# Kernel optimization log

Hardware: AMD Instinct MI355X
Metric: run time of the kernel (lower is better)

The kernel has to match this reference:

```python
import jax, jax.numpy as jnp
import numpy as np

B, T, C = 48, 200, 53          # batch, timepoints, ICA components
E, H, A = 32, 64, 64            # embed dim, GRU hidden dim, attention hidden dim
C2 = C * C                      # 2809
E1 = round(0.05 * C2)           # gta_embed out = 140
E2 = round(0.5 * C2)            # gta_attend hidden = 1404
O = 2                           # output classes
BN_EPS = 1e-5


def setup_inputs() -> dict:
    key = jax.random.key(0)
    ks = jax.random.split(key, 24)
    n = lambda k, shape, s: jax.random.normal(k, shape, dtype=jnp.float32) * s
    return {
        "x": jax.random.normal(ks[0], (B, T, C), dtype=jnp.float32),
        "emb_w": n(ks[1], (E,), 0.3), "emb_b": n(ks[2], (E,), 0.1),
        "w_ih": n(ks[3], (3 * H, E), 0.12), "w_hh": n(ks[4], (3 * H, H), 0.12),
        "b_ih": n(ks[5], (3 * H,), 0.05), "b_hh": n(ks[6], (3 * H,), 0.05),
        "wq": n(ks[7], (A, H), 0.12), "bq": n(ks[8], (A,), 0.05),
        "wk": n(ks[9], (A, H), 0.12), "bk": n(ks[10], (A,), 0.05),
        "wv": n(ks[11], (H, H), 0.12), "bv": n(ks[12], (H,), 0.05),
        "u0": jax.random.normal(ks[13], (H,), dtype=jnp.float32),
        "w_g1": n(ks[14], (E1, C2), 0.02), "b_g1": n(ks[15], (E1,), 0.02),
        "bn_g": jnp.ones((E1,), jnp.float32), "bn_b": jnp.zeros((E1,), jnp.float32),
        "w_g2": n(ks[16], (E2, E1), 0.05), "b_g2": n(ks[17], (E2,), 0.05),
        "w_g3": n(ks[18], (1, E2), 0.02), "b_g3": n(ks[19], (1,), 0.02),
        "w_clf": n(ks[20], (O, C2), 0.02), "b_clf": jnp.zeros((O,), jnp.float32),
    }


def _normalize(v, eps=1e-12):
    return v / (jnp.linalg.norm(v) + eps)


def _gru_cell(x, h, w_ih, w_hh, b_ih, b_hh):
    # torch GRU cell math. x:(N,E) h:(N,H)
    gi = x @ w_ih.T + b_ih
    gh = h @ w_hh.T + b_hh
    i_r, i_z, i_n = jnp.split(gi, 3, axis=-1)
    h_r, h_z, h_n = jnp.split(gh, 3, axis=-1)
    r = jax.nn.sigmoid(i_r + h_r)
    z = jax.nn.sigmoid(i_z + h_z)
    n = jnp.tanh(i_n + r * h_n)
    return (1.0 - z) * n + z * h


def _forward(x, emb_w, emb_b, w_ih, w_hh, b_ih, b_hh, wq, bq, wk, bk, wv, bv, u0,
             w_g1, b_g1, bn_g, bn_b, w_g2, b_g2, w_g3, b_g3, w_clf, b_clf):
    Bs, Ts, Cs = x.shape
    Hd = wv.shape[0]
    # single shared Linear(1,E) embedding: (B,T,C) -> (T,B,C,E) for scan
    emb = x[..., None] * emb_w + emb_b
    emb = jnp.transpose(emb, (1, 0, 2, 3))
    h0 = jnp.zeros((Bs * Cs, Hd), x.dtype)

    def step(carry, emb_t):
        h, u = carry
        hg = _gru_cell(emb_t.reshape(Bs * Cs, -1), h, w_ih, w_hh, b_ih, b_hh)
        hb = hg.reshape(Bs, Cs, Hd)
        # spectral_norm on value weight: 5 power iterations (no_grad, as torch)
        v = None
        for _ in range(5):
            v = _normalize(wv.T @ u)
            u = _normalize(wv @ v)
        u = jax.lax.stop_gradient(u)
        v = jax.lax.stop_gradient(v)
        sigma = u @ (wv @ v)
        q = hb @ wq.T + bq          # (B,C,A)
        k = hb @ wk.T + bk          # (B,C,A)
        val = hb @ (wv / sigma).T + bv  # (B,C,H)
        scores = jnp.einsum('bia,bja->bij', q, k)  # (B,C,C)
        # eigenvalue-based spectral normalization (detached: track_grads=False)
        ev = jnp.linalg.eigvals(jax.lax.stop_gradient(scores))
        m = jnp.max(jnp.abs(ev), axis=1)[:, None, None].astype(x.dtype)
        attn = scores / m
        h_new = jnp.einsum('bij,bjh->bih', attn, val).reshape(Bs * Cs, Hd)
        return (h_new, u), attn

    (_, _), aligns = jax.lax.scan(step, (h0, u0), emb)  # aligns: (T,B,C,C)
    align = jnp.transpose(aligns, (1, 0, 2, 3))         # (B,T,C,C)
    Aflat = align.reshape(Bs, Ts, Cs * Cs)

    # gta_attention over the time axis
    xr = Aflat * Aflat.mean(axis=1, keepdims=True)
    flat = xr.reshape(Bs * Ts, Cs * Cs)
    e = flat @ w_g1.T + b_g1
    mu = e.mean(axis=0)
    var = e.var(axis=0)  # biased, as torch BatchNorm1d (training)
    e = jax.nn.relu((e - mu) / jnp.sqrt(var + BN_EPS) * bn_g + bn_b)
    a = jax.nn.relu(e @ w_g2.T + b_g2) @ w_g3.T + b_g3   # (B*T,1)
    a = jax.nn.softmax(a.reshape(Bs, Ts), axis=1)
    dnc = (Aflat * a[..., None]).sum(axis=1)             # (B,C*C)
    logits = dnc @ w_clf.T + b_clf
    return logits, dnc.reshape(Bs, Cs, Cs), align


def reference(x, emb_w, emb_b, w_ih, w_hh, b_ih, b_hh, wq, bq, wk, bk, wv, bv, u0,
              w_g1, b_g1, bn_g, bn_b, w_g2, b_g2, w_g3, b_g3, w_clf, b_clf):
    return _forward(x, emb_w, emb_b, w_ih, w_hh, b_ih, b_hh, wq, bq, wk, bk, wv, bv, u0,
                    w_g1, b_g1, bn_g, bn_b, w_g2, b_g2, w_g3, b_g3, w_clf, b_clf)
```

## Files before the change

kernel.cpp:

```cpp
#include <hip/hip_runtime.h>
#include <hip/hip_bf16.h>
#include <math.h>

#define B_  48
#define T_  200
#define C_  53
#define H_  64
#define C2_ 2809
#define E1_ 140
#define E2_ 1404
#define TS  60

typedef long long i64;

struct __align__(16) F4 { float v[4]; };

__device__ __forceinline__ float wredsum(float v){
  #pragma unroll
  for (int o = 32; o > 0; o >>= 1) v += __shfl_xor(v, o);
  return v;
}
__device__ __forceinline__ float sigm(float x){ return 1.f/(1.f + __expf(-x)); }
__device__ __forceinline__ float tanhx(float x){
  float a = fabsf(x);
  float e = __expf(-2.f*a);
  float t = (1.f - e)/(1.f + e);
  return copysignf(t, x);
}

__device__ __forceinline__ void eig_mm(const float* __restrict__ X, float* __restrict__ Y,
                                       int r0, int c0, float inv,
                                       float& essq, float& etrc){
  float ea0[4] = {0.f,0.f,0.f,0.f};
  float ea1[4] = {0.f,0.f,0.f,0.f};
  for (int kq = 0; kq < 13; kq++){
    int k4 = kq*4;
    F4 a0 = *(const F4*)&X[(r0+0)*TS + k4];
    F4 a1 = *(const F4*)&X[(r0+1)*TS + k4];
    F4 b0 = *(const F4*)&X[(k4+0)*TS + c0];
    F4 b1 = *(const F4*)&X[(k4+1)*TS + c0];
    F4 b2 = *(const F4*)&X[(k4+2)*TS + c0];
    F4 b3 = *(const F4*)&X[(k4+3)*TS + c0];
    #pragma unroll
    for (int ci = 0; ci < 4; ci++){
      ea0[ci] += a0.v[0]*b0.v[ci] + a0.v[1]*b1.v[ci] + a0.v[2]*b2.v[ci] + a0.v[3]*b3.v[ci];
      ea1[ci] += a1.v[0]*b0.v[ci] + a1.v[1]*b1.v[ci] + a1.v[2]*b2.v[ci] + a1.v[3]*b3.v[ci];
    }
  }
  {
    float a0 = X[(r0+0)*TS + 52], a1 = X[(r0+1)*TS + 52];
    F4 bb = *(const F4*)&X[52*TS + c0];
    #pragma unroll
    for (int ci = 0; ci < 4; ci++){ ea0[ci] += a0*bb.v[ci]; ea1[ci] += a1*bb.v[ci]; }
  }
  F4 o0, o1;
  #pragma unroll
  for (int ci = 0; ci < 4; ci++){
    o0.v[ci] = ea0[ci]*inv;
    o1.v[ci] = ea1[ci]*inv;
    essq += o0.v[ci]*o0.v[ci] + o1.v[ci]*o1.v[ci];
  }
  if (r0   >= c0 && r0   < c0+4) etrc += o0.v[r0-c0];
  if (r0+1 >= c0 && r0+1 < c0+4) etrc += o1.v[r0+1-c0];
  *(F4*)&Y[(r0+0)*TS + c0] = o0;
  *(F4*)&Y[(r0+1)*TS + c0] = o1;
}

#define OFF_SIGMA 0
#define OFF_WHHT  200
#define OFF_WZV   12488
#define OFF_WUV   20680
#define OFF_P     20812
#define OFF_R0    21004
#define OFF_MM    21196
#define OFF_M2    25292
#define OFF_M4    29388
#define OFF_M5    33484
#define OFF_AMEAN 37580
#define OFF_E     172412
#define OFF_CA    1516412
#define OFF_CB    1516552
#define OFF_APRE  1516692
#define OFF_A     1526292
#define OFF_G2T   1535892

__global__ void k_prep1(const float* __restrict__ w_hh, const float* __restrict__ wq,
                        const float* __restrict__ wk, const float* __restrict__ wv,
                        const float* __restrict__ w_ih, const float* __restrict__ emb_w,
                        const float* __restrict__ emb_b, const float* __restrict__ b_ih,
                        const float* __restrict__ bq, const float* __restrict__ bk,
                        const float* __restrict__ w_g2,
                        float* whhT, float* wzv, float* wuv, float* g2t,
                        float* p, float* r0){
  int idx0 = blockIdx.x*blockDim.x + threadIdx.x;
  int stride = gridDim.x*blockDim.x;
  for (int i = idx0; i < 64*192; i += stride){
    int kk = i/192, g = i%192;
    whhT[i] = w_hh[g*64 + kk];
  }
  for (int i = idx0; i < 8192; i += stride){
    int h = i >> 7, a = i & 127;
    if (a < 64){
      float g = 0.f;
      for (int m = 0; m < 64; m++) g += wq[m*64 + h]*wk[m*64 + a];
      wzv[i] = g;
    } else {
      wzv[i] = wv[(a-64)*64 + h];
    }
  }
  for (int i = idx0; i < 129; i += stride){
    if (i < 64){
      float s = 0.f;
      for (int m = 0; m < 64; m++) s += wq[m*64 + i]*bk[m];
      wuv[i] = s;
    } else if (i < 128){
      int h = i - 64;
      float s = 0.f;
      for (int m = 0; m < 64; m++) s += wk[m*64 + h]*bq[m];
      wuv[i] = s;
    } else {
      float s = 0.f;
      for (int m = 0; m < 64; m++) s += bq[m]*bk[m];
      wuv[128] = s;
    }
  }
  for (int i = idx0; i < 140*1404; i += stride){ int k = i/1404, n = i%1404; g2t[i] = w_g2[n*140+k]; }
  for (int i = idx0; i < 192; i += stride){
    float s1 = 0.f, s2 = 0.f;
    for (int e = 0; e < 32; e++){ float w = w_ih[i*32+e]; s1 += w*emb_w[e]; s2 += w*emb_b[e]; }
    p[i] = s1; r0[i] = s2 + b_ih[i];
  }
}

__global__ void k_prep2(const float* __restrict__ wv, const float* __restrict__ u0,
                        float* Wm, float* Wm2, float* Wm4, float* Wm5, float* sigma){
  int r = threadIdx.x;
  for (int c = 0; c < 64; c++){
    float s = 0.f;
    for (int k = 0; k < 64; k++) s += wv[r*64+k]*wv[c*64+k];
    Wm[r*64+c] = s;
  }
  __syncthreads();
  for (int c = 0; c < 64; c++){
    float s = 0.f;
    for (int k = 0; k < 64; k++) s += Wm[r*64+k]*Wm[k*64+c];
    Wm2[r*64+c] = s;
  }
  __syncthreads();
  for (int c = 0; c < 64; c++){
    float s = 0.f;
    for (int k = 0; k < 64; k++) s += Wm2[r*64+k]*Wm2[k*64+c];
    Wm4[r*64+c] = s;
  }
  __syncthreads();
  for (int c = 0; c < 64; c++){
    float s = 0.f;
    for (int k = 0; k < 64; k++) s += Wm4[r*64+k]*Wm[k*64+c];
    Wm5[r*64+c] = s;
  }
  __syncthreads();
  __shared__ float su[64];
  su[r] = u0[r];
  __syncthreads();
  for (int t = 0; t < T_; t++){
    float z = 0.f, w = 0.f;
    for (int k = 0; k < 64; k++){ float uk = su[k]; z += Wm4[r*64+k]*uk; w += Wm5[r*64+k]*uk; }
    float nw = wredsum(w*w);
    float zw = wredsum(z*w);
    float sg = sqrtf(nw / fmaxf(zw, 1e-35f));
    if (r == 0) sigma[t] = sg;
    float wn = w * (1.f/sqrtf(fmaxf(nw, 1e-35f)));
    __syncthreads();
    su[r] = wn;
    __syncthreads();
  }
}

__global__ __launch_bounds__(512, 1) void k_scan(
    const float* __restrict__ x, const float* __restrict__ b_hh,
    const float* __restrict__ bv,
    const float* __restrict__ whhT, const float* __restrict__ wzv,
    const float* __restrict__ wuv,
    const float* __restrict__ wp, const float* __restrict__ wr0,
    const float* __restrict__ sigma, float* __restrict__ outAL){
  __shared__ __align__(16) float L[19056];
  float* Rh  = L;
  float* R4  = L + 3840;
  float* R3  = L + 7680;
  float* R2  = L + 11520;
  float* R1  = L + 14912;
  float* Lp  = L + 18272;
  float* Lr0 = L + 18464;
  float* Lbh = L + 18656;
  float* Lbv = L + 18848;
  float* Lrq = L + 18912;
  float* Lrk = L + 18968;
  float* Lsc = L + 19024;
  int tid = threadIdx.x;
  int b = blockIdx.x;

  for (int i = tid; i < 192; i += 512){ Lp[i] = wp[i]; Lr0[i] = wr0[i]; Lbh[i] = b_hh[i]; }
  for (int i = tid; i < 64; i += 512) Lbv[i] = bv[i];
  for (int i = tid; i < 18272; i += 512) L[i] = 0.f;
  __syncthreads();

  int ct4 = tid >> 4, jt4 = tid & 15;
  int c0g = ct4*4, j0g = jt4*4;
  int it14 = tid/14, jt14 = tid%14;
  int i0s = it14*4, j0s = jt14*4;
  int ctq = tid >> 5, gtq = tid & 31;
  int c0q = ctq*4, g0q = gtq*4;
  int erg = tid/14, ecg = tid%14;
  int er0 = erg*2, ec0 = ecg*4;

  const float c0v = wuv[128];

  for (int t = 0; t < T_; t++){
    if (tid < 32) Lsc[tid] = 0.f;
    if (tid < 224){
      float gacc[3][4][4];
      #pragma unroll
      for (int g = 0; g < 3; g++)
        #pragma unroll
        for (int ji = 0; ji < 4; ji++){
          float bb = Lbh[g*64 + j0g + ji];
          #pragma unroll
          for (int ci = 0; ci < 4; ci++) gacc[g][ji][ci] = bb;
        }
      for (int kk = 0; kk < 64; kk++){
        F4 hv = *(F4*)&Rh[kk*TS + c0g];
        F4 w0 = *(const F4*)&whhT[kk*192 + j0g];
        F4 w1 = *(const F4*)&whhT[kk*192 + 64 + j0g];
        F4 w2 = *(const F4*)&whhT[kk*192 + 128 + j0g];
        #pragma unroll
        for (int ji = 0; ji < 4; ji++)
          #pragma unroll
          for (int ci = 0; ci < 4; ci++){
            gacc[0][ji][ci] += hv.v[ci]*w0.v[ji];
            gacc[1][ji][ci] += hv.v[ci]*w1.v[ji];
            gacc[2][ji][ci] += hv.v[ci]*w2.v[ji];
          }
      }
      float xv[4];
      #pragma unroll
      for (int ci = 0; ci < 4; ci++){
        int c = c0g + ci;
        xv[ci] = (c < C_) ? x[(i64)(b*T_ + t)*C_ + c] : 0.f;
      }
      F4 p0 = *(F4*)&Lp[j0g], p1 = *(F4*)&Lp[64+j0g], p2 = *(F4*)&Lp[128+j0g];
      F4 q0 = *(F4*)&Lr0[j0g], q1 = *(F4*)&Lr0[64+j0g], q2 = *(F4*)&Lr0[128+j0g];
      #pragma unroll
      for (int ji = 0; ji < 4; ji++){
        F4 hold = *(F4*)&Rh[(j0g+ji)*TS + c0g];
        F4 o;
        #pragma unroll
        for (int ci = 0; ci < 4; ci++){
          float rr = sigm(xv[ci]*p0.v[ji] + q0.v[ji] + gacc[0][ji][ci]);
          float zz = sigm(xv[ci]*p1.v[ji] + q1.v[ji] + gacc[1][ji][ci]);
          float nn = tanhx(xv[ci]*p2.v[ji] + q2.v[ji] + rr*gacc[2][ji][ci]);
          float hg = (1.f - zz)*nn + zz*hold.v[ci];
          o.v[ci] = (c0g + ci < C_) ? hg : 0.f;
        }
        *(F4*)&R4[(j0g+ji)*TS + c0g] = o;
      }
    }
    __syncthreads();
    if (tid < 448){
      float acc[4][4];
      #pragma unroll
      for (int gi = 0; gi < 4; gi++)
        #pragma unroll
        for (int ci = 0; ci < 4; ci++) acc[gi][ci] = 0.f;
      for (int kk = 0; kk < 64; kk++){
        F4 a = *(F4*)&R4[kk*TS + c0q];
        F4 w = *(const F4*)&wzv[kk*128 + g0q];
        #pragma unroll
        for (int gi = 0; gi < 4; gi++)
          #pragma unroll
          for (int ci = 0; ci < 4; ci++) acc[gi][ci] += a.v[ci]*w.v[gi];
      }
      if (g0q < 64){
        #pragma unroll
        for (int gi = 0; gi < 4; gi++){
          F4 o;
          #pragma unroll
          for (int ci = 0; ci < 4; ci++) o.v[ci] = acc[gi][ci];
          *(F4*)&R3[(g0q+gi)*TS + c0q] = o;
        }
      } else {
        float invs = 1.f/sigma[t];
        int a0i = g0q - 64;
        #pragma unroll
        for (int ci = 0; ci < 4; ci++){
          int c = c0q + ci;
          if (c < C_){
            F4 o;
            #pragma unroll
            for (int gi = 0; gi < 4; gi++) o.v[gi] = acc[gi][ci]*invs + Lbv[a0i+gi];
            *(F4*)&R2[c*64 + a0i] = o;
          }
        }
      }
    } else if (tid < 504){
      int u = tid - 448;
      float rq = 0.f, rk = 0.f;
      if (u < C_){
        for (int h = 0; h < 64; h++){
          float hv = R4[h*TS + u];
          rq += hv*wuv[h];
          rk += hv*wuv[64+h];
        }
      }
      if (u < 56){ Lrq[u] = rq; Lrk[u] = rk; }
    }
    __syncthreads();
    {
      float sacc[4][4];
      float ssq = 0.f, trc = 0.f;
      if (tid < 196){
        #pragma unroll
        for (int ii = 0; ii < 4; ii++)
          #pragma unroll
          for (int jj = 0; jj < 4; jj++){
            int i = i0s + ii, j = j0s + jj;
            sacc[ii][jj] = (i < C_ && j < C_) ? (Lrq[i] + Lrk[j] + c0v) : 0.f;
          }
        for (int aq = 0; aq < 16; aq++){
          int a4 = aq*4;
          F4 qa0 = *(F4*)&R3[(a4+0)*TS + i0s];
          F4 qa1 = *(F4*)&R3[(a4+1)*TS + i0s];
          F4 qa2 = *(F4*)&R3[(a4+2)*TS + i0s];
          F4 qa3 = *(F4*)&R3[(a4+3)*TS + i0s];
          F4 kb0 = *(F4*)&R4[(a4+0)*TS + j0s];
          F4 kb1 = *(F4*)&R4[(a4+1)*TS + j0s];
          F4 kb2 = *(F4*)&R4[(a4+2)*TS + j0s];
          F4 kb3 = *(F4*)&R4[(a4+3)*TS + j0s];
          #pragma unroll
          for (int ii = 0; ii < 4; ii++)
            #pragma unroll
            for (int jj = 0; jj < 4; jj++)
              sacc[ii][jj] += qa0.v[ii]*kb0.v[jj] + qa1.v[ii]*kb1.v[jj]
                            + qa2.v[ii]*kb2.v[jj] + qa3.v[ii]*kb3.v[jj];
        }
        #pragma unroll
        for (int ii = 0; ii < 4; ii++){
          int i = i0s + ii;
          if (i < C_){
            F4 o;
            #pragma unroll
            for (int jj = 0; jj < 4; jj++){
              o.v[jj] = sacc[ii][jj];
              ssq += sacc[ii][jj]*sacc[ii][jj];
            }
            *(F4*)&R1[i*TS + j0s] = o;
          }
        }
        if (it14 == jt14){
          #pragma unroll
          for (int u = 0; u < 4; u++) if (i0s + u < C_) trc += sacc[u][u];
        }
      }
      ssq = wredsum(ssq); trc = wredsum(trc);
      if ((tid & 63) == 0){
        if (ssq != 0.f) atomicAdd(&Lsc[0], ssq);
        if (trc != 0.f) atomicAdd(&Lsc[1], trc);
      }
    }
    __syncthreads();
    {
      float inv0 = 1.f/fmaxf(Lsc[0], 1e-35f);
      float essq = 0.f, etrc = 0.f;
      if (tid < 378) eig_mm(R1, R3, er0, ec0, inv0, essq, etrc);
      essq = wredsum(essq); etrc = wredsum(etrc);
      if ((tid & 63) == 0){
        if (essq != 0.f) atomicAdd(&Lsc[2], essq);
        if (etrc != 0.f) atomicAdd(&Lsc[3], etrc);
      }
    }
    __syncthreads();
    float Gacc = 0.f, prevest = 1e30f, est = 0.f;
    int cnt = 0;
    float pssq = fmaxf(Lsc[0], 1e-35f), ptr1 = Lsc[1];
    float* Xb = R3; float* Yb = R4;
    for (int j = 2; j <= 13; j++){
      float sj = fmaxf(Lsc[2*(j-1)], 1e-35f);
      float tj = Lsc[2*(j-1)+1];
      int J = j - 2;
      float t1n = ptr1/sqrtf(pssq);
      float t2n = tj;
      float disc = 2.f*t2n - t1n*t1n;
      float rq = (disc >= 0.f) ? 0.5f*(fabsf(t1n) + sqrtf(disc))
                               : sqrtf(fmaxf(0.5f*(t1n*t1n - t2n), 1e-30f));
      rq = fminf(fmaxf(rq, 0.02f), 1.5f);
      est = Gacc + ldexpf(0.5f*log2f(pssq) + log2f(rq), -J);
      if (fabsf(est - prevest) < 1e-4f) cnt++; else cnt = 0;
      prevest = est;
      Gacc += ldexpf(log2f(pssq), -(J+1));
      if ((J >= 5 && cnt >= 1) || j == 13) break;
      pssq = sj; ptr1 = tj;
      {
        float inv = 1.f/sj;
        float essq = 0.f, etrc = 0.f;
        if (tid < 378) eig_mm(Xb, Yb, er0, ec0, inv, essq, etrc);
        essq = wredsum(essq); etrc = wredsum(etrc);
        if ((tid & 63) == 0){
          if (essq != 0.f) atomicAdd(&Lsc[2*j], essq);
          if (etrc != 0.f) atomicAdd(&Lsc[2*j+1], etrc);
        }
      }
      { float* tp = Xb; Xb = Yb; Yb = tp; }
      __syncthreads();
    }
    float invm = exp2f(-est);
    if (tid < 224){
      float hraw0[4] = {0.f,0.f,0.f,0.f};
      float hraw1[4] = {0.f,0.f,0.f,0.f};
      float hraw2[4] = {0.f,0.f,0.f,0.f};
      float hraw3[4] = {0.f,0.f,0.f,0.f};
      for (int kq = 0; kq < 13; kq++){
        int k4 = kq*4;
        F4 a0 = *(F4*)&R1[(c0g+0)*TS + k4];
        F4 a1 = *(F4*)&R1[(c0g+1)*TS + k4];
        F4 a2 = *(F4*)&R1[(c0g+2)*TS + k4];
        F4 a3 = *(F4*)&R1[(c0g+3)*TS + k4];
        F4 b0 = *(F4*)&R2[(k4+0)*64 + j0g];
        F4 b1 = *(F4*)&R2[(k4+1)*64 + j0g];
        F4 b2 = *(F4*)&R2[(k4+2)*64 + j0g];
        F4 b3 = *(F4*)&R2[(k4+3)*64 + j0g];
        #pragma unroll
        for (int jj = 0; jj < 4; jj++){
          hraw0[jj] += a0.v[0]*b0.v[jj] + a0.v[1]*b1.v[jj] + a0.v[2]*b2.v[jj] + a0.v[3]*b3.v[jj];
          hraw1[jj] += a1.v[0]*b0.v[jj] + a1.v[1]*b1.v[jj] + a1.v[2]*b2.v[jj] + a1.v[3]*b3.v[jj];
          hraw2[jj] += a2.v[0]*b0.v[jj] + a2.v[1]*b1.v[jj] + a2.v[2]*b2.v[jj] + a2.v[3]*b3.v[jj];
          hraw3[jj] += a3.v[0]*b0.v[jj] + a3.v[1]*b1.v[jj] + a3.v[2]*b2.v[jj] + a3.v[3]*b3.v[jj];
        }
      }
      {
        const int k = 52;
        float a0 = R1[(c0g+0)*TS + k], a1 = R1[(c0g+1)*TS + k];
        float a2 = R1[(c0g+2)*TS + k], a3 = R1[(c0g+3)*TS + k];
        F4 bb = *(F4*)&R2[k*64 + j0g];
        #pragma unroll
        for (int jj = 0; jj < 4; jj++){
          hraw0[jj] += a0*bb.v[jj];
          hraw1[jj] += a1*bb.v[jj];
          hraw2[jj] += a2*bb.v[jj];
          hraw3[jj] += a3*bb.v[jj];
        }
      }
      #pragma unroll
      for (int jj = 0; jj < 4; jj++){
        F4 o;
        o.v[0] = (c0g + 0 < C_) ? hraw0[jj]*invm : 0.f;
        o.v[1] = (c0g + 1 < C_) ? hraw1[jj]*invm : 0.f;
        o.v[2] = (c0g + 2 < C_) ? hraw2[jj]*invm : 0.f;
        o.v[3] = (c0g + 3 < C_) ? hraw3[jj]*invm : 0.f;
        *(F4*)&Rh[(j0g+jj)*TS + c0g] = o;
      }
    } else if (tid < 420){
      int u = tid - 224;
      int i0 = (u/14)*4, j0 = (u%14)*4;
      float* ALrow = outAL + (i64)(b*T_ + t)*C2_;
      #pragma unroll
      for (int ii = 0; ii < 4; ii++){
        int i = i0 + ii;
        if (i < C_){
          F4 s = *(F4*)&R1[i*TS + j0];
          #pragma unroll
          for (int jj = 0; jj < 4; jj++){
            int j = j0 + jj;
            if (j < C_) ALrow[i*C_ + j] = s.v[jj]*invm;
          }
        }
      }
    }
    __syncthreads();
  }
}

__global__ void k_amean(const float* __restrict__ AL, float* __restrict__ amean){
  int b = blockIdx.x/11, ch = blockIdx.x%11;
  int c2 = ch*256 + threadIdx.x;
  if (c2 >= C2_) return;
  float acc = 0.f;
  for (int t = 0; t < T_; t++)
    acc += AL[(i64)(b*T_ + t)*C2_ + c2];
  amean[(i64)b*C2_ + c2] = acc*(1.f/(float)T_);
}

__global__ __launch_bounds__(128) void k_gemm1(const float* __restrict__ AL,
                                               const float* __restrict__ amean,
                                               const float* __restrict__ w_g1,
                                               float* __restrict__ e){
  __shared__ __align__(16) float At[64][68];
  __shared__ __align__(16) float Bt[64][148];
  int mt = blockIdx.x >> 2, ks = blockIdx.x & 3;
  int tid = threadIdx.x;
  float acc[8][12];
  #pragma unroll
  for (int ri = 0; ri < 8; ri++)
    #pragma unroll
    for (int ci = 0; ci < 12; ci++) acc[ri][ci] = 0.f;
  int rg = tid/12, cg = tid%12;
  int r0 = rg*8, cc0 = cg*12;
  for (int kb = 0; kb < 11; kb++){
    int k0 = (ks*11 + kb)*64;
    for (int idx = tid; idx < 4096; idx += 128){
      int r = idx >> 6, i = idx & 63;
      int kk = k0 + i;
      int row = mt*64 + r, bb = row/T_;
      float v = 0.f;
      if (kk < C2_) v = AL[(i64)row*C2_ + kk]*amean[(i64)bb*C2_ + kk];
      At[i][r] = v;
    }
    for (int idx = tid; idx < 9216; idx += 128){
      int c = idx >> 6, i = idx & 63;
      int kk = k0 + i;
      float v = 0.f;
      if (c < E1_ && kk < C2_) v = w_g1[(i64)c*C2_ + kk];
      Bt[i][c] = v;
    }
    __syncthreads();
    if (tid < 96){
      for (int i = 0; i < 64; i++){
        F4 a0 = *(F4*)&At[i][r0]; F4 a1 = *(F4*)&At[i][r0+4];
        F4 b0 = *(F4*)&Bt[i][cc0]; F4 b1 = *(F4*)&Bt[i][cc0+4]; F4 b2 = *(F4*)&Bt[i][cc0+8];
        #pragma unroll
        for (int ri = 0; ri < 8; ri++){
          float av = (ri < 4) ? a0.v[ri] : a1.v[ri-4];
          #pragma unroll
          for (int ci = 0; ci < 12; ci++){
            float bv = (ci < 4) ? b0.v[ci] : (ci < 8) ? b1.v[ci-4] : b2.v[ci-8];
            acc[ri][ci] += av*bv;
          }
        }
      }
    }
    __syncthreads();
  }
  if (tid < 96){
    #pragma unroll
    for (int ri = 0; ri < 8; ri++)
      #pragma unroll
      for (int ci = 0; ci < 12; ci++){
        int c = cc0 + ci;
        if (c < E1_) atomicAdd(&e[(i64)(mt*64 + r0 + ri)*E1_ + c], acc[ri][ci]);
      }
  }
}

__global__ void k_bnstats(const float* __restrict__ e, const float* __restrict__ bn_g,
                          const float* __restrict__ bn_b, float* cA, float* cB){
  __shared__ float s1a[256], s2a[256];
  int c = blockIdx.x, tid = threadIdx.x;
  float s1 = 0.f, s2 = 0.f;
  for (int row = tid; row < B_*T_; row += 256){
    float v = e[(i64)row*E1_ + c];
    s1 += v; s2 += v*v;
  }
  s1a[tid] = s1; s2a[tid] = s2; __syncthreads();
  for (int s = 128; s > 0; s >>= 1){
    if (tid < s){ s1a[tid] += s1a[tid+s]; s2a[tid] += s2a[tid+s]; }
    __syncthreads();
  }
  if (tid == 0){
    float n = (float)(B_*T_);
    float mu = s1a[0]/n;
    float var = s2a[0]/n - mu*mu;
    float a = bn_g[c]/sqrtf(var + 1e-5f);
    cA[c] = a; cB[c] = bn_b[c] - mu*a;
  }
}

__global__ __launch_bounds__(128) void k_gemm2(const float* __restrict__ e,
                                               const float* __restrict__ cA, const float* __restrict__ cB,
                                               const float* __restrict__ g2t,
                                               const float* __restrict__ b_g2, const float* __restrict__ w_g3,
                                               float* __restrict__ apre){
  __shared__ __align__(16) float At2[140][68];
  int mt = blockIdx.x/30, nc = blockIdx.x%30;
  int tid = threadIdx.x;
  int nbase = nc*48;
  for (int idx = tid; idx < 64*140; idx += 128){
    int r = idx/140, k = idx - r*140;
    float v = e[(i64)(mt*64 + r)*E1_ + k]*cA[k] + cB[k];
    At2[k][r] = fmaxf(v, 0.f);
  }
  __syncthreads();
  if (tid < 96){
    int rg = tid/6, ng = tid%6;
    int r0 = rg*4, n0 = nbase + ng*8;
    float acc[4][8];
    #pragma unroll
    for (int ri = 0; ri < 4; ri++)
      #pragma unroll
      for (int ni = 0; ni < 8; ni++) acc[ri][ni] = 0.f;
    for (int k = 0; k < E1_; k++){
      F4 a = *(F4*)&At2[k][r0];
      float bvv[8];
      if (n0 + 8 <= E2_){
        F4 b0 = *(const F4*)&g2t[(i64)k*E2_ + n0];
        F4 b1 = *(const F4*)&g2t[(i64)k*E2_ + n0 + 4];
        #pragma unroll
        for (int u = 0; u < 4; u++){ bvv[u] = b0.v[u]; bvv[u+4] = b1.v[u]; }
      } else {
        #pragma unroll
        for (int ni = 0; ni < 8; ni++){ int n = n0+ni; bvv[ni] = (n < E2_) ? g2t[(i64)k*E2_ + n] : 0.f; }
      }
      #pragma unroll
      for (int ri = 0; ri < 4; ri++)
        #pragma unroll
        for (int ni = 0; ni < 8; ni++) acc[ri][ni] += a.v[ri]*bvv[ni];
    }
    #pragma unroll
    for (int ri = 0; ri < 4; ri++){
      float s = 0.f;
      #pragma unroll
      for (int ni = 0; ni < 8; ni++){
        int n = n0 + ni;
        if (n < E2_){
          float a2 = acc[ri][ni] + b_g2[n];
          if (a2 > 0.f) s += a2*w_g3[n];
        }
      }
      atomicAdd(&apre[mt*64 + r0 + ri], s);
    }
  }
}

__global__ void k_soft(const float* __restrict__ apre, const float* __restrict__ b_clf,
                       float* __restrict__ wa, float* __restrict__ out){
  __shared__ float sr[256];
  int b = blockIdx.x, tid = threadIdx.x;
  float v = (tid < T_) ? apre[b*T_ + tid] : -3.4e38f;
  sr[tid] = v; __syncthreads();
  for (int s = 128; s > 0; s >>= 1){ if (tid < s) sr[tid] = fmaxf(sr[tid], sr[tid+s]); __syncthreads(); }
  float mx = sr[0]; __syncthreads();
  float ev = (tid < T_) ? __expf(v - mx) : 0.f;
  sr[tid] = ev; __syncthreads();
  for (int s = 128; s > 0; s >>= 1){ if (tid < s) sr[tid] += sr[tid+s]; __syncthreads(); }
  float den = sr[0];
  if (tid < T_) wa[b*T_ + tid] = ev/den;
  if (b == 0 && tid < 2*B_) out[tid] = b_clf[tid & 1];
}

__global__ void k_dnc(const float* __restrict__ AL, const float* __restrict__ wa,
                      const float* __restrict__ w_clf, float* __restrict__ out){
  int b = blockIdx.x/11, ch = blockIdx.x%11;
  int c2 = ch*256 + threadIdx.x;
  float acc = 0.f;
  if (c2 < C2_){
    for (int t = 0; t < T_; t++)
      acc += AL[(i64)(b*T_ + t)*C2_ + c2]*wa[b*T_ + t];
    out[96 + (i64)b*C2_ + c2] = acc;
  }
  float p0 = (c2 < C2_) ? acc*w_clf[c2]        : 0.f;
  float p1 = (c2 < C2_) ? acc*w_clf[C2_ + c2]  : 0.f;
  p0 = wredsum(p0); p1 = wredsum(p1);
  if ((threadIdx.x & 63) == 0){
    atomicAdd(&out[b*2 + 0], p0);
    atomicAdd(&out[b*2 + 1], p1);
  }
}

extern "C" void kernel_launch(void* const* d_in, const int* in_sizes, int n_in,
                              void* d_out, int out_size, void* d_ws, size_t ws_size,
                              hipStream_t stream){
  const float* x     = (const float*)d_in[0];
  const float* emb_w = (const float*)d_in[1];
  const float* emb_b = (const float*)d_in[2];
  const float* w_ih  = (const float*)d_in[3];
  const float* w_hh  = (const float*)d_in[4];
  const float* b_ih  = (const float*)d_in[5];
  const float* b_hh  = (const float*)d_in[6];
  const float* wq    = (const float*)d_in[7];
  const float* bq    = (const float*)d_in[8];
  const float* wk    = (const float*)d_in[9];
  const float* bk    = (const float*)d_in[10];
  const float* wv_in = (const float*)d_in[11];
  const float* bv    = (const float*)d_in[12];
  const float* u0    = (const float*)d_in[13];
  const float* w_g1  = (const float*)d_in[14];
  const float* bn_g  = (const float*)d_in[16];
  const float* bn_b  = (const float*)d_in[17];
  const float* w_g2  = (const float*)d_in[18];
  const float* b_g2  = (const float*)d_in[19];
  const float* w_g3  = (const float*)d_in[20];
  const float* w_clf = (const float*)d_in[22];
  const float* b_clf = (const float*)d_in[23];
  float* out = (float*)d_out;
  float* W = (float*)d_ws;

  float* wsig   = W + OFF_SIGMA;
  float* whhT   = W + OFF_WHHT;
  float* wzv    = W + OFF_WZV;
  float* wuv    = W + OFF_WUV;
  float* wp     = W + OFF_P;
  float* wr0    = W + OFF_R0;
  float* wM     = W + OFF_MM;
  float* wM2    = W + OFF_M2;
  float* wM4    = W + OFF_M4;
  float* wM5    = W + OFF_M5;
  float* wamean = W + OFF_AMEAN;
  float* we     = W + OFF_E;
  float* wcA    = W + OFF_CA;
  float* wcB    = W + OFF_CB;
  float* wapre  = W + OFF_APRE;
  float* wa     = W + OFF_A;
  float* wg2t   = W + OFF_G2T;

  float* outAL = out + 96 + (i64)B_*C2_;

  hipMemsetAsync(we, 0, (size_t)(B_*T_)*E1_*sizeof(float), stream);
  hipMemsetAsync(wapre, 0, (size_t)(B_*T_)*sizeof(float), stream);

  k_prep1<<<96, 256, 0, stream>>>(w_hh, wq, wk, wv_in, w_ih, emb_w, emb_b, b_ih, bq, bk,
                                  w_g2, whhT, wzv, wuv, wg2t, wp, wr0);
  k_prep2<<<1, 64, 0, stream>>>(wv_in, u0, wM, wM2, wM4, wM5, wsig);
  k_scan<<<B_, 512, 0, stream>>>(x, b_hh, bv, whhT, wzv, wuv, wp, wr0, wsig, outAL);
  k_amean<<<B_*11, 256, 0, stream>>>(outAL, wamean);
  k_gemm1<<<600, 128, 0, stream>>>(outAL, wamean, w_g1, we);
  k_bnstats<<<E1_, 256, 0, stream>>>(we, bn_g, bn_b, wcA, wcB);
  k_gemm2<<<150*30, 128, 0, stream>>>(we, wcA, wcB, wg2t, b_g2, w_g3, wapre);
  k_soft<<<B_, 256, 0, stream>>>(wapre, b_clf, wa, out);
  k_dnc<<<B_*11, 256, 0, stream>>>(outAL, wa, w_clf, out);
}
```

Measured before the change: 9.682 ms.

## Stage GRU weights in LDS, fuse time-mean into scan, loosen convergence

Copies the transposed GRU hidden weights into shared memory so the recurrent matvec reads LDS instead of global memory on every timestep. Accumulates the per-batch time mean of the alignment matrices inside the scan kernel, removing the separate amean kernel and its re-read of the alignment output. Also simplifies the trace accumulation and lets the iterative eigen-estimate loop stop one iteration earlier, which trades some accuracy margin for fewer matrix multiplies per step. Shared memory use grows to about 137 KB per block.

```diff
diff --git a/kernel.cpp b/kernel.cpp
--- a/kernel.cpp
+++ b/kernel.cpp
@@ -182,26 +182,31 @@
     const float* __restrict__ whhT, const float* __restrict__ wzv,
     const float* __restrict__ wuv,
     const float* __restrict__ wp, const float* __restrict__ wr0,
-    const float* __restrict__ sigma, float* __restrict__ outAL){
-  __shared__ __align__(16) float L[19056];
-  float* Rh  = L;
-  float* R4  = L + 3840;
-  float* R3  = L + 7680;
-  float* R2  = L + 11520;
-  float* R1  = L + 14912;
-  float* Lp  = L + 18272;
-  float* Lr0 = L + 18464;
-  float* Lbh = L + 18656;
-  float* Lbv = L + 18848;
-  float* Lrq = L + 18912;
-  float* Lrk = L + 18968;
-  float* Lsc = L + 19024;
+    const float* __restrict__ sigma, float* __restrict__ outAL,
+    float* __restrict__ wamean){
+  __shared__ __align__(16) float L[34160];
+  float* Lw  = L;
+  float* Rh  = L + 12288;
+  float* R4  = L + 16128;
+  float* R3  = L + 19968;
+  float* R2  = L + 23808;
+  float* R1  = L + 27200;
+  float* Lp  = L + 30560;
+  float* Lr0 = L + 30752;
+  float* Lbh = L + 30944;
+  float* Lbv = L + 31136;
+  float* Lrq = L + 31200;
+  float* Lrk = L + 31256;
+  float* Lsc = L + 31312;
+  float* Lmean = L + 31344;
   int tid = threadIdx.x;
   int b = blockIdx.x;
 
+  for (int i = tid; i < 3072; i += 512) *(F4*)&Lw[i*4] = *(const F4*)&whhT[i*4];
   for (int i = tid; i < 192; i += 512){ Lp[i] = wp[i]; Lr0[i] = wr0[i]; Lbh[i] = b_hh[i]; }
   for (int i = tid; i < 64; i += 512) Lbv[i] = bv[i];
-  for (int i = tid; i < 18272; i += 512) L[i] = 0.f;
+  for (int i = tid; i < 18272; i += 512) L[12288 + i] = 0.f;
+  for (int i = tid; i < 2816; i += 512) Lmean[i] = 0.f;
   __syncthreads();
 
   int ct4 = tid >> 4, jt4 = tid & 15;
@@ -229,9 +234,9 @@
         }
       for (int kk = 0; kk < 64; kk++){
         F4 hv = *(F4*)&Rh[kk*TS + c0g];
-        F4 w0 = *(const F4*)&whhT[kk*192 + j0g];
-        F4 w1 = *(const F4*)&whhT[kk*192 + 64 + j0g];
-        F4 w2 = *(const F4*)&whhT[kk*192 + 128 + j0g];
+        F4 w0 = *(const F4*)&Lw[kk*192 + j0g];
+        F4 w1 = *(const F4*)&Lw[kk*192 + 64 + j0g];
+        F4 w2 = *(const F4*)&Lw[kk*192 + 128 + j0g];
         #pragma unroll
         for (int ji = 0; ji < 4; ji++)
           #pragma unroll
@@ -353,11 +358,8 @@
               ssq += sacc[ii][jj]*sacc[ii][jj];
             }
             *(F4*)&R1[i*TS + j0s] = o;
+            if (j0s <= i && i < j0s + 4) trc += sacc[ii][i - j0s];
           }
-        }
-        if (it14 == jt14){
-          #pragma unroll
-          for (int u = 0; u < 4; u++) if (i0s + u < C_) trc += sacc[u][u];
         }
       }
       ssq = wredsum(ssq); trc = wredsum(trc);
@@ -396,7 +398,7 @@
       if (fabsf(est - prevest) < 1e-4f) cnt++; else cnt = 0;
       prevest = est;
       Gacc += ldexpf(log2f(pssq), -(J+1));
-      if ((J >= 5 && cnt >= 1) || j == 13) break;
+      if ((J >= 4 && cnt >= 1) || j == 13) break;
       pssq = sj; ptr1 = tj;
       {
         float inv = 1.f/sj;
@@ -468,24 +470,20 @@
           F4 s = *(F4*)&R1[i*TS + j0];
           #pragma unroll
           for (int jj = 0; jj < 4; jj++){
-            int j = j0 + jj;
-            if (j < C_) ALrow[i*C_ + j] = s.v[jj]*invm;
+            int jc = j0 + jj;
+            if (jc < C_){
+              float v = s.v[jj]*invm;
+              ALrow[i*C_ + jc] = v;
+              Lmean[i*C_ + jc] += v;
+            }
           }
         }
       }
     }
     __syncthreads();
   }
-}
-
-__global__ void k_amean(const float* __restrict__ AL, float* __restrict__ amean){
-  int b = blockIdx.x/11, ch = blockIdx.x%11;
-  int c2 = ch*256 + threadIdx.x;
-  if (c2 >= C2_) return;
-  float acc = 0.f;
-  for (int t = 0; t < T_; t++)
-    acc += AL[(i64)(b*T_ + t)*C2_ + c2];
-  amean[(i64)b*C2_ + c2] = acc*(1.f/(float)T_);
+  for (int i = tid; i < C2_; i += 512)
+    wamean[(i64)b*C2_ + i] = Lmean[i]*(1.f/(float)T_);
 }
 
 __global__ __launch_bounds__(128) void k_gemm1(const float* __restrict__ AL,
@@ -717,8 +715,7 @@
   k_prep1<<<96, 256, 0, stream>>>(w_hh, wq, wk, wv_in, w_ih, emb_w, emb_b, b_ih, bq, bk,
                                   w_g2, whhT, wzv, wuv, wg2t, wp, wr0);
   k_prep2<<<1, 64, 0, stream>>>(wv_in, u0, wM, wM2, wM4, wM5, wsig);
-  k_scan<<<B_, 512, 0, stream>>>(x, b_hh, bv, whhT, wzv, wuv, wp, wr0, wsig, outAL);
-  k_amean<<<B_*11, 256, 0, stream>>>(outAL, wamean);
+  k_scan<<<B_, 512, 0, stream>>>(x, b_hh, bv, whhT, wzv, wuv, wp, wr0, wsig, outAL, wamean);
   k_gemm1<<<600, 128, 0, stream>>>(outAL, wamean, w_g1, we);
   k_bnstats<<<E1_, 256, 0, stream>>>(we, bn_g, bn_b, wcA, wcB);
   k_gemm2<<<150*30, 128, 0, stream>>>(we, wcA, wcB, wg2t, b_g2, w_g3, wapre);
```

After: 10.25 ms. 1.06x slower.

## Fuse time-mean into scan, loosen eigen iteration cutoff, simplify trace accumulation

Applied to the files above, without the earlier changes.

The per-batch time mean of the alignment maps is now accumulated in shared memory inside the scan kernel and written out at the end, which removes the separate k_amean kernel and its second read of the full alignment tensor. The convergence test for the iterative spectral-norm estimate now allows an earlier exit (J>=4 instead of J>=5), which saves squaring iterations per timestep but may cost accuracy. The trace accumulation is also folded into the store loop. Shared memory use grows by about 11 KB.

```diff
diff --git a/kernel.cpp b/kernel.cpp
--- a/kernel.cpp
+++ b/kernel.cpp
@@ -182,8 +182,9 @@
     const float* __restrict__ whhT, const float* __restrict__ wzv,
     const float* __restrict__ wuv,
     const float* __restrict__ wp, const float* __restrict__ wr0,
-    const float* __restrict__ sigma, float* __restrict__ outAL){
-  __shared__ __align__(16) float L[19056];
+    const float* __restrict__ sigma, float* __restrict__ outAL,
+    float* __restrict__ wamean){
+  __shared__ __align__(16) float L[21872];
   float* Rh  = L;
   float* R4  = L + 3840;
   float* R3  = L + 7680;
@@ -196,12 +197,14 @@
   float* Lrq = L + 18912;
   float* Lrk = L + 18968;
   float* Lsc = L + 19024;
+  float* Lmean = L + 19056;
   int tid = threadIdx.x;
   int b = blockIdx.x;
 
   for (int i = tid; i < 192; i += 512){ Lp[i] = wp[i]; Lr0[i] = wr0[i]; Lbh[i] = b_hh[i]; }
   for (int i = tid; i < 64; i += 512) Lbv[i] = bv[i];
   for (int i = tid; i < 18272; i += 512) L[i] = 0.f;
+  for (int i = tid; i < 2816; i += 512) Lmean[i] = 0.f;
   __syncthreads();
 
   int ct4 = tid >> 4, jt4 = tid & 15;
@@ -353,11 +356,8 @@
               ssq += sacc[ii][jj]*sacc[ii][jj];
             }
             *(F4*)&R1[i*TS + j0s] = o;
+            if (j0s <= i && i < j0s + 4) trc += sacc[ii][i - j0s];
           }
-        }
-        if (it14 == jt14){
-          #pragma unroll
-          for (int u = 0; u < 4; u++) if (i0s + u < C_) trc += sacc[u][u];
         }
       }
       ssq = wredsum(ssq); trc = wredsum(trc);
@@ -396,7 +396,7 @@
       if (fabsf(est - prevest) < 1e-4f) cnt++; else cnt = 0;
       prevest = est;
       Gacc += ldexpf(log2f(pssq), -(J+1));
-      if ((J >= 5 && cnt >= 1) || j == 13) break;
+      if ((J >= 4 && cnt >= 1) || j == 13) break;
       pssq = sj; ptr1 = tj;
       {
         float inv = 1.f/sj;
@@ -468,24 +468,20 @@
           F4 s = *(F4*)&R1[i*TS + j0];
           #pragma unroll
           for (int jj = 0; jj < 4; jj++){
-            int j = j0 + jj;
-            if (j < C_) ALrow[i*C_ + j] = s.v[jj]*invm;
+            int jc = j0 + jj;
+            if (jc < C_){
+              float v = s.v[jj]*invm;
+              ALrow[i*C_ + jc] = v;
+              Lmean[i*C_ + jc] += v;
+            }
           }
         }
       }
     }
     __syncthreads();
   }
-}
-
-__global__ void k_amean(const float* __restrict__ AL, float* __restrict__ amean){
-  int b = blockIdx.x/11, ch = blockIdx.x%11;
-  int c2 = ch*256 + threadIdx.x;
-  if (c2 >= C2_) return;
-  float acc = 0.f;
-  for (int t = 0; t < T_; t++)
-    acc += AL[(i64)(b*T_ + t)*C2_ + c2];
-  amean[(i64)b*C2_ + c2] = acc*(1.f/(float)T_);
+  for (int i = tid; i < C2_; i += 512)
+    wamean[(i64)b*C2_ + i] = Lmean[i]*(1.f/(float)T_);
 }
 
 __global__ __launch_bounds__(128) void k_gemm1(const float* __restrict__ AL,
@@ -717,8 +713,7 @@
   k_prep1<<<96, 256, 0, stream>>>(w_hh, wq, wk, wv_in, w_ih, emb_w, emb_b, b_ih, bq, bk,
                                   w_g2, whhT, wzv, wuv, wg2t, wp, wr0);
   k_prep2<<<1, 64, 0, stream>>>(wv_in, u0, wM, wM2, wM4, wM5, wsig);
-  k_scan<<<B_, 512, 0, stream>>>(x, b_hh, bv, whhT, wzv, wuv, wp, wr0, wsig, outAL);
-  k_amean<<<B_*11, 256, 0, stream>>>(outAL, wamean);
+  k_scan<<<B_, 512, 0, stream>>>(x, b_hh, bv, whhT, wzv, wuv, wp, wr0, wsig, outAL, wamean);
   k_gemm1<<<600, 128, 0, stream>>>(outAL, wamean, w_g1, we);
   k_bnstats<<<E1_, 256, 0, stream>>>(we, bn_g, bn_b, wcA, wcB);
   k_gemm2<<<150*30, 128, 0, stream>>>(we, wcA, wcB, wg2t, b_g2, w_g3, wapre);
```

Result: slower. 11.06 ms (+14.2%).
